# Kernel tuning notes

Measured on AMD Instinct MI355X. Metric: run time of the kernel, lower is better.

Reference implementation:

```python
import jax, jax.numpy as jnp
import numpy as np

EPS = 1e-6
NUM_HEADS = 8


def setup_inputs() -> dict:
    key0 = jax.random.key(0)
    ks = jax.random.split(key0, 8)
    N, B, C, HW = 900, 8, 256, 1156

    def lin(k):
        kw, kb = jax.random.split(k)
        W = jax.random.normal(kw, (C, C), jnp.float32) * 0.02
        b = jax.random.normal(kb, (C,), jnp.float32) * 0.02
        return W, b

    Wq, bq = lin(ks[0])
    Wk, bk = lin(ks[1])
    Wv, bv = lin(ks[2])
    Wo, bo = lin(ks[3])
    query = jax.random.normal(ks[4], (N, B, C), jnp.float32)
    key = jax.random.normal(ks[5], (HW, B, C), jnp.float32)
    query_pos = jax.random.normal(ks[6], (N, B, C), jnp.float32)
    key_pos = jax.random.normal(ks[7], (HW, B, C), jnp.float32)
    return dict(query=query, key=key, query_pos=query_pos, key_pos=key_pos,
                Wq=Wq, bq=bq, Wk=Wk, bk=bk, Wv=Wv, bv=bv, Wo=Wo, bo=bo)


def reference(query, key, query_pos, key_pos, Wq, bq, Wk, bk, Wv, bv, Wo, bo):
    # Faithful port of LinearCrossAttention.forward (value=None -> key,
    # identity=None -> query, batch_first=False, dropout inactive).
    # NOTE: the original permutes to (B, seq, head, head_dim) but then applies
    # cumsum(dim=2) / einsums along axis 2, i.e. over the HEAD axis; we
    # reproduce that exactly.
    N, B, C = query.shape
    HW = key.shape[0]
    H = NUM_HEADS
    D = C // H

    q = (query @ Wq.T + bq) + query_pos          # (N,B,C)
    k = (key @ Wk.T + bk) + key_pos              # (HW,B,C)
    v = key @ Wv.T + bv                          # (HW,B,C)

    q = jnp.transpose(q.reshape(N, B, H, D), (1, 0, 2, 3))    # (B,N,H,D)
    k = jnp.transpose(k.reshape(HW, B, H, D), (1, 0, 2, 3))   # (B,HW,H,D)
    v = jnp.transpose(v.reshape(HW, B, H, D), (1, 0, 2, 3))   # (B,HW,H,D)

    q = jax.nn.sigmoid(q)
    k = jax.nn.sigmoid(k)

    if HW > N:  # pad queries along the sequence axis
        q = jnp.concatenate([q, jnp.zeros((B, HW - N, H, D), q.dtype)], axis=1)

    dot = lambda a, b: jnp.sum(a * b, axis=-1)   # 'nhld,nhld->nhl'

    sink_incoming = 1.0 / dot(q + EPS, jnp.cumsum(k, axis=2) + EPS)   # (B,HW,H)
    source_outgoing = 1.0 / dot(k + EPS, jnp.cumsum(q, axis=2) + EPS)
    normal = (jnp.arange(H, dtype=q.dtype) + 1.0)[None, None, :]       # (1,1,H)
    sink_incoming = sink_incoming * normal
    source_outgoing = source_outgoing * normal

    conserved_sink = dot(q + EPS, jnp.cumsum(k * source_outgoing[..., None], axis=2) + EPS) / normal
    conserved_source = dot(k + EPS, jnp.cumsum(q * sink_incoming[..., None], axis=2) + EPS) / normal
    conserved_source = jnp.clip(conserved_source, -1.0, 1.0)

    sink_allocation = jax.nn.sigmoid(conserved_sink)
    conserved_source = jnp.exp(conserved_source)
    source_competition = conserved_source / jnp.cumsum(conserved_source, axis=-1) * normal

    # causal_dot_product with cumsum over axis 2 (head axis in this layout)
    qs = q * (sink_incoming[..., None] / normal[..., None])            # (B,HW,H,D)
    kv = jnp.cumsum(jnp.einsum('blhd,blhm->blhdm', k, v * source_competition[..., None]), axis=2)
    qkv = jnp.einsum('blhd,blhdm->blhm', qs, kv)                       # (B,HW,H,D)

    out = (qkv * sink_allocation[..., None])[:, :N]                    # (B,N,H,D)
    out = jnp.swapaxes(out, 1, 2).reshape(B, N, C)                     # matches torch transpose(1,2).reshape
    out = out @ Wo.T + bo
    out = jnp.swapaxes(out, 0, 1)                                      # (N,B,C)
    return query + out
```

## Files before the change

kernel.cpp:

```cpp
#include <hip/hip_runtime.h>
#include <math.h>

#define EPSV 1e-6f
constexpr int N_ = 900, B_ = 8, C_ = 256, H_ = 8, D_ = 32;
constexpr int M_TOT = N_ * B_;
constexpr int BM  = 32;
constexpr int NBLK = M_TOT / BM;
constexpr int VS  = 272;
constexpr int OFF_AQ = 65536;
constexpr int OFF_AK = 81920;
constexpr int OFF_Q  = 98304;
constexpr int OFF_K  = OFF_Q + BM * VS * 2;
constexpr int OFF_V  = OFF_K + BM * VS * 2;
constexpr int LDS1   = OFF_V + BM * VS * 2;
constexpr int LDS2   = 81920;

typedef __attribute__((ext_vector_type(8))) short short8;
typedef __attribute__((ext_vector_type(4))) float f32x4;
typedef __attribute__((ext_vector_type(2))) float f32x2;
typedef __attribute__((ext_vector_type(2))) unsigned short us2;

__device__ __forceinline__ unsigned short f2bf(float f) {
    unsigned int u = __float_as_uint(f);
    return (unsigned short)((u + 0x7FFFu + ((u >> 16) & 1u)) >> 16);
}
__device__ __forceinline__ float bf2f(unsigned short u) {
    return __uint_as_float(((unsigned int)u) << 16);
}
__device__ __forceinline__ int swz(int row, int kElem) {
    int b = (row << 9) + (kElem << 1);
    return b ^ ((row & 7) << 4);
}
__device__ __forceinline__ float red16(float v) {
    v += __shfl_xor(v, 1); v += __shfl_xor(v, 2);
    v += __shfl_xor(v, 4); v += __shfl_xor(v, 8);
    return v;
}

__global__ __launch_bounds__(256)
void pack_w(const float* __restrict__ Wq, const float* __restrict__ Wk,
            const float* __restrict__ Wv, const float* __restrict__ Wo,
            unsigned short* __restrict__ wbf)
{
    const int i = (blockIdx.x * 256 + threadIdx.x) * 8;
    const float* src = (i < 65536) ? Wq : (i < 131072) ? Wk
                     : (i < 196608) ? Wv : Wo;
    const int off = i & 65535;
    const float4 a = *reinterpret_cast<const float4*>(src + off);
    const float4 b = *reinterpret_cast<const float4*>(src + off + 4);
    short8 p;
    p[0]=(short)f2bf(a.x); p[1]=(short)f2bf(a.y);
    p[2]=(short)f2bf(a.z); p[3]=(short)f2bf(a.w);
    p[4]=(short)f2bf(b.x); p[5]=(short)f2bf(b.y);
    p[6]=(short)f2bf(b.z); p[7]=(short)f2bf(b.w);
    *reinterpret_cast<short8*>(wbf + i) = p;
}

__device__ __forceinline__ void stageW32(const unsigned short* Wmat, int kkElem,
                                         char* wbufLds, int cw, int lane)
{
    #pragma unroll
    for (int n = 0; n < 4; ++n) {
        const int L  = n * 1024 + lane * 16;
        const int cl = L >> 7;
        const int kb = (L & 127) ^ ((cl & 7) << 4);
        const char* src = (const char*)Wmat + (size_t)(cw + cl) * 512
                        + kkElem * 2 + kb;
        __builtin_amdgcn_global_load_lds(
            (const __attribute__((address_space(1))) unsigned int*)src,
            (__attribute__((address_space(3))) unsigned int*)(wbufLds + n * 1024),
            16, 0, 0);
    }
}

__device__ __forceinline__ void step_mm32(const unsigned char* At, const char* wb,
                                          int kkA, int lrow, int kg8,
                                          f32x4 acc[2][2])
{
    #pragma unroll
    for (int kh = 0; kh < 2; ++kh) {
        const short8 a0 = *reinterpret_cast<const short8*>(At + swz(lrow,      kkA + kh*32 + kg8));
        const short8 a1 = *reinterpret_cast<const short8*>(At + swz(16 + lrow, kkA + kh*32 + kg8));
        #pragma unroll
        for (int j = 0; j < 2; ++j) {
            const int cl = j*16 + lrow;
            const short8 bfr = *reinterpret_cast<const short8*>(
                wb + cl*128 + ((kh*64 + kg8*2) ^ ((cl & 7) << 4)));
            acc[0][j] = __builtin_amdgcn_mfma_f32_16x16x32_bf16(a0, bfr, acc[0][j], 0, 0, 0);
            acc[1][j] = __builtin_amdgcn_mfma_f32_16x16x32_bf16(a1, bfr, acc[1][j], 0, 0, 0);
        }
    }
}

__global__ __launch_bounds__(512)
void fused_qkva(const float* __restrict__ query, const float* __restrict__ key,
                const float* __restrict__ qpos,  const float* __restrict__ kpos,
                const unsigned short* __restrict__ wbf,
                const float* __restrict__ bq, const float* __restrict__ bk,
                const float* __restrict__ bv,
                unsigned short* __restrict__ abf)
{
    extern __shared__ char smem[];
    char* Wb = smem;
    unsigned char* Aq = (unsigned char*)(smem + OFF_AQ);
    unsigned char* Ak = (unsigned char*)(smem + OFF_AK);
    unsigned short* q_sb = (unsigned short*)(smem + OFF_Q);
    unsigned short* k_sb = (unsigned short*)(smem + OFF_K);
    unsigned short* v_sb = (unsigned short*)(smem + OFF_V);

    const int tid = threadIdx.x;
    const int r0  = blockIdx.x * BM;
    const int wave = tid >> 6, lane = tid & 63;
    const int cw = wave * 32;
    char* mywb = Wb + wave * 8192;

    stageW32(wbf, 0, mywb, cw, lane);

    {
        const int trow = tid >> 5, k0 = (tid & 31) * 8;
        #pragma unroll
        for (int i = 0; i < 2; ++i) {
            const int row = trow + i * 16;
            const float* xr = query + (size_t)(r0 + row) * C_ + k0;
            const float4 a0 = *reinterpret_cast<const float4*>(xr);
            const float4 a1 = *reinterpret_cast<const float4*>(xr + 4);
            short8 pa;
            pa[0]=(short)f2bf(a0.x); pa[1]=(short)f2bf(a0.y);
            pa[2]=(short)f2bf(a0.z); pa[3]=(short)f2bf(a0.w);
            pa[4]=(short)f2bf(a1.x); pa[5]=(short)f2bf(a1.y);
            pa[6]=(short)f2bf(a1.z); pa[7]=(short)f2bf(a1.w);
            *reinterpret_cast<short8*>(Aq + swz(row, k0)) = pa;
            const float* kr = key + (size_t)(r0 + row) * C_ + k0;
            const float4 b0 = *reinterpret_cast<const float4*>(kr);
            const float4 b1 = *reinterpret_cast<const float4*>(kr + 4);
            short8 pb;
            pb[0]=(short)f2bf(b0.x); pb[1]=(short)f2bf(b0.y);
            pb[2]=(short)f2bf(b0.z); pb[3]=(short)f2bf(b0.w);
            pb[4]=(short)f2bf(b1.x); pb[5]=(short)f2bf(b1.y);
            pb[6]=(short)f2bf(b1.z); pb[7]=(short)f2bf(b1.w);
            *reinterpret_cast<short8*>(Ak + swz(row, k0)) = pb;
        }
    }

    const int lrow = lane & 15, kg8 = (lane >> 4) * 8;
    const int crow0 = (lane >> 4) * 4, ccol = lane & 15;

    float qp[16], kp[16], bqv[2], bkv[2], bvv[2];
    #pragma unroll
    for (int j = 0; j < 2; ++j) {
        const int ch = cw + j*16 + ccol;
        bqv[j] = bq[ch]; bkv[j] = bk[ch]; bvv[j] = bv[ch];
        #pragma unroll
        for (int rh = 0; rh < 2; ++rh)
            #pragma unroll
            for (int r_ = 0; r_ < 4; ++r_) {
                const int gr = r0 + rh*16 + crow0 + r_;
                qp[j*8+rh*4+r_] = qpos[(size_t)gr * C_ + ch];
                kp[j*8+rh*4+r_] = kpos[(size_t)gr * C_ + ch];
            }
    }

    __syncthreads();

    f32x4 qacc[2][2] = {}; f32x4 kacc[2][2] = {}; f32x4 vacc[2][2] = {};

    #pragma unroll
    for (int st = 0; st < 12; ++st) {
        if (st < 11) {
            const int nx = st + 1;
            stageW32(wbf + (nx >> 2) * 65536, (nx & 3) * 64,
                     mywb + (nx & 1) * 4096, cw, lane);
            asm volatile("s_waitcnt vmcnt(4)" ::: "memory");
        } else {
            asm volatile("s_waitcnt vmcnt(0)" ::: "memory");
        }

        const char* wb = mywb + (st & 1) * 4096;
        const int kkA = (st & 3) * 64;
        if (st < 4)      step_mm32(Aq, wb, kkA, lrow, kg8, qacc);
        else if (st < 8) step_mm32(Ak, wb, kkA, lrow, kg8, kacc);
        else             step_mm32(Ak, wb, kkA, lrow, kg8, vacc);

        if (st == 3) {
            #pragma unroll
            for (int j = 0; j < 2; ++j) {
                const int ch = cw + j*16 + ccol;
                #pragma unroll
                for (int rh = 0; rh < 2; ++rh)
                    #pragma unroll
                    for (int r_ = 0; r_ < 4; ++r_) {
                        float v = qacc[rh][j][r_] + bqv[j] + qp[j*8+rh*4+r_];
                        q_sb[(rh*16+crow0+r_)*VS + ch] = f2bf(1.f/(1.f+expf(-v)));
                    }
            }
        }
        if (st == 7) {
            #pragma unroll
            for (int j = 0; j < 2; ++j) {
                const int ch = cw + j*16 + ccol;
                #pragma unroll
                for (int rh = 0; rh < 2; ++rh)
                    #pragma unroll
                    for (int r_ = 0; r_ < 4; ++r_) {
                        float v = kacc[rh][j][r_] + bkv[j] + kp[j*8+rh*4+r_];
                        k_sb[(rh*16+crow0+r_)*VS + ch] = f2bf(1.f/(1.f+expf(-v)));
                    }
            }
        }
        if (st == 11) {
            #pragma unroll
            for (int j = 0; j < 2; ++j) {
                const int ch = cw + j*16 + ccol;
                #pragma unroll
                for (int rh = 0; rh < 2; ++rh)
                    #pragma unroll
                    for (int r_ = 0; r_ < 4; ++r_)
                        v_sb[(rh*16+crow0+r_)*VS + ch] =
                            f2bf(vacc[rh][j][r_] + bvv[j]);
            }
        }
    }

    __syncthreads();

    {
        const int loc = tid >> 4, tt = tid & 15, d0 = tt * 2;
        const int gr = r0 + loc;
        const int nn = gr >> 3, bb = gr & 7;
        const unsigned short* qr = q_sb + loc * VS + d0;
        const unsigned short* kr = k_sb + loc * VS + d0;
        const unsigned short* vr = v_sb + loc * VS + d0;
        f32x2 qh[8], kh[8], vh[8];
        #pragma unroll
        for (int h = 0; h < 8; ++h) {
            const us2 tq = *reinterpret_cast<const us2*>(qr + (h << 5));
            const us2 tk = *reinterpret_cast<const us2*>(kr + (h << 5));
            const us2 tv = *reinterpret_cast<const us2*>(vr + (h << 5));
            qh[h][0] = bf2f(tq[0]); qh[h][1] = bf2f(tq[1]);
            kh[h][0] = bf2f(tk[0]); kh[h][1] = bf2f(tk[1]);
            vh[h][0] = bf2f(tv[0]); vh[h][1] = bf2f(tv[1]);
        }

        float ir1[8], so_[8];
        {
            f32x2 ck = {0,0}, cq = {0,0};
            #pragma unroll
            for (int h = 0; h < 8; ++h) {
                float p1 = 0.f, p2 = 0.f;
                #pragma unroll
                for (int j = 0; j < 2; ++j) {
                    ck[j] += kh[h][j]; cq[j] += qh[h][j];
                    p1 += (qh[h][j] + EPSV) * (ck[j] + EPSV);
                    p2 += (kh[h][j] + EPSV) * (cq[j] + EPSV);
                }
                p1 = red16(p1); p2 = red16(p2);
                ir1[h] = 1.f / p1;
                so_[h] = (float)(h+1) / p2;
            }
        }
        float salloc[8], scomp[8];
        {
            f32x2 c2 = {0,0}, c3 = {0,0};
            float css = 0.f;
            #pragma unroll
            for (int h = 0; h < 8; ++h) {
                const float sih = (float)(h+1) * ir1[h];
                float p3 = 0.f, p4 = 0.f;
                #pragma unroll
                for (int j = 0; j < 2; ++j) {
                    c2[j] += kh[h][j] * so_[h];
                    c3[j] += qh[h][j] * sih;
                    p3 += (qh[h][j] + EPSV) * (c2[j] + EPSV);
                    p4 += (kh[h][j] + EPSV) * (c3[j] + EPSV);
                }
                p3 = red16(p3); p4 = red16(p4);
                const float inv_n = 1.f / (float)(h+1);
                salloc[h] = 1.f / (1.f + expf(-p3 * inv_n));
                const float consrc = fminf(1.f, fmaxf(-1.f, p4 * inv_n));
                const float cs = expf(consrc);
                css += cs;
                scomp[h] = cs / css * (float)(h+1);
            }
        }
        #pragma unroll
        for (int h = 0; h < 8; ++h) {
            f32x2 qs2, a2 = {0,0};
            #pragma unroll
            for (int j = 0; j < 2; ++j) qs2[j] = qh[h][j] * ir1[h];
            #pragma unroll
            for (int h2 = 0; h2 <= h; ++h2) {
                float p = 0.f;
                #pragma unroll
                for (int j = 0; j < 2; ++j) p += qs2[j] * kh[h2][j];
                p = red16(p);
                const float w = p * scomp[h2];
                #pragma unroll
                for (int j = 0; j < 2; ++j) a2[j] += w * vh[h2][j];
            }
            us2 o;
            o[0] = f2bf(a2[0] * salloc[h]);
            o[1] = f2bf(a2[1] * salloc[h]);
            *reinterpret_cast<us2*>(abf + (size_t)bb*(H_*N_*D_) + (size_t)h*(N_*D_)
                                        + (size_t)nn*D_ + d0) = o;
        }
    }
}

__global__ __launch_bounds__(512)
void outproj(const unsigned short* __restrict__ abf,
             const unsigned short* __restrict__ wbf,
             const float* __restrict__ bo,
             const float* __restrict__ query,
             float* __restrict__ out)
{
    extern __shared__ char smem[];
    char* Wb = smem;
    unsigned char* As = (unsigned char*)(smem + 65536);
    const int tid = threadIdx.x;
    const int r0  = blockIdx.x * BM;
    const int wave = tid >> 6, lane = tid & 63;
    const int cw = wave * 32;
    char* mywb = Wb + wave * 8192;
    const unsigned short* Wo = wbf + 3*65536;

    stageW32(Wo, 0, mywb, cw, lane);

    {
        const int trow = tid >> 5, k0 = (tid & 31) * 8;
        #pragma unroll
        for (int i = 0; i < 2; ++i) {
            const int row = trow + i * 16;
            const int gr = r0 + row;
            const int nn = gr >> 3, bb = gr & 7;
            const short8 p = *reinterpret_cast<const short8*>(
                abf + (size_t)bb * (N_*C_) + (size_t)nn * C_ + k0);
            *reinterpret_cast<short8*>(As + swz(row, k0)) = p;
        }
    }

    const int lrow = lane & 15, kg8 = (lane >> 4) * 8;
    const int crow0 = (lane >> 4) * 4, ccol = lane & 15;

    float bov[2], qres[16];
    #pragma unroll
    for (int j = 0; j < 2; ++j) {
        const int ch = cw + j*16 + ccol;
        bov[j] = bo[ch];
        #pragma unroll
        for (int rh = 0; rh < 2; ++rh)
            #pragma unroll
            for (int r_ = 0; r_ < 4; ++r_)
                qres[j*8+rh*4+r_] =
                    query[(size_t)(r0 + rh*16 + crow0 + r_) * C_ + ch];
    }

    __syncthreads();

    f32x4 acc[2][2] = {};
    #pragma unroll
    for (int sp = 0; sp < 4; ++sp) {
        if (sp < 3) {
            stageW32(Wo, (sp+1)*64, mywb + ((sp+1) & 1) * 4096, cw, lane);
            asm volatile("s_waitcnt vmcnt(4)" ::: "memory");
        } else {
            asm volatile("s_waitcnt vmcnt(0)" ::: "memory");
        }
        step_mm32(As, mywb + (sp & 1) * 4096, sp*64, lrow, kg8, acc);
    }

    #pragma unroll
    for (int j = 0; j < 2; ++j) {
        const int ch = cw + j*16 + ccol;
        #pragma unroll
        for (int rh = 0; rh < 2; ++rh)
            #pragma unroll
            for (int r_ = 0; r_ < 4; ++r_) {
                const size_t g = (size_t)(r0 + rh*16 + crow0 + r_) * C_ + ch;
                out[g] = acc[rh][j][r_] + bov[j] + qres[j*8+rh*4+r_];
            }
    }
}

extern "C" void kernel_launch(void* const* d_in, const int* in_sizes, int n_in,
                              void* d_out, int out_size, void* d_ws, size_t ws_size,
                              hipStream_t stream)
{
    const float* query = (const float*)d_in[0];
    const float* key   = (const float*)d_in[1];
    const float* qpos  = (const float*)d_in[2];
    const float* kpos  = (const float*)d_in[3];
    const float* Wq = (const float*)d_in[4];  const float* bq = (const float*)d_in[5];
    const float* Wk = (const float*)d_in[6];  const float* bk = (const float*)d_in[7];
    const float* Wv = (const float*)d_in[8];  const float* bv = (const float*)d_in[9];
    const float* Wo = (const float*)d_in[10]; const float* bo = (const float*)d_in[11];

    unsigned short* wbf = (unsigned short*)d_ws;
    unsigned short* abf = wbf + 4*65536;
    float* out = (float*)d_out;

    pack_w<<<128, 256, 0, stream>>>(Wq, Wk, Wv, Wo, wbf);
    fused_qkva<<<NBLK, 512, LDS1, stream>>>(query, key, qpos, kpos, wbf,
                                            bq, bk, bv, abf);
    outproj<<<NBLK, 512, LDS2, stream>>>(abf, wbf, bo, query, out);
}
```

Baseline: 34.26 us.

## Drop weight pre-pack kernel; stream fp32 weights and convert to bf16 in-loop

Removes the separate pack_w launch that converted all four weight matrices to bf16, and instead streams fp32 weights directly into LDS and converts them to bf16 right before each MFMA. This saves one kernel launch and the write and re-read of the packed weights. In exchange, every block re-converts weights redundantly, fetches twice the weight bytes per k-step, and the K loop runs twice as many stages with half the work per stage.

Result: slower. 46.77 us (+36.5%).

```diff
diff --git a/kernel.cpp b/kernel.cpp
--- a/kernel.cpp
+++ b/kernel.cpp
@@ -37,35 +37,15 @@
     return v;
 }
 
-__global__ __launch_bounds__(256)
-void pack_w(const float* __restrict__ Wq, const float* __restrict__ Wk,
-            const float* __restrict__ Wv, const float* __restrict__ Wo,
-            unsigned short* __restrict__ wbf)
-{
-    const int i = (blockIdx.x * 256 + threadIdx.x) * 8;
-    const float* src = (i < 65536) ? Wq : (i < 131072) ? Wk
-                     : (i < 196608) ? Wv : Wo;
-    const int off = i & 65535;
-    const float4 a = *reinterpret_cast<const float4*>(src + off);
-    const float4 b = *reinterpret_cast<const float4*>(src + off + 4);
-    short8 p;
-    p[0]=(short)f2bf(a.x); p[1]=(short)f2bf(a.y);
-    p[2]=(short)f2bf(a.z); p[3]=(short)f2bf(a.w);
-    p[4]=(short)f2bf(b.x); p[5]=(short)f2bf(b.y);
-    p[6]=(short)f2bf(b.z); p[7]=(short)f2bf(b.w);
-    *reinterpret_cast<short8*>(wbf + i) = p;
-}
-
-__device__ __forceinline__ void stageW32(const unsigned short* Wmat, int kkElem,
-                                         char* wbufLds, int cw, int lane)
+__device__ __forceinline__ void stageW32f(const float* Wmat, int kk32,
+                                          char* wbufLds, int cw, int lane)
 {
     #pragma unroll
     for (int n = 0; n < 4; ++n) {
         const int L  = n * 1024 + lane * 16;
         const int cl = L >> 7;
         const int kb = (L & 127) ^ ((cl & 7) << 4);
-        const char* src = (const char*)Wmat + (size_t)(cw + cl) * 512
-                        + kkElem * 2 + kb;
+        const char* src = (const char*)(Wmat + (size_t)(cw + cl) * C_ + kk32) + kb;
         __builtin_amdgcn_global_load_lds(
             (const __attribute__((address_space(1))) unsigned int*)src,
             (__attribute__((address_space(3))) unsigned int*)(wbufLds + n * 1024),
@@ -73,29 +53,33 @@
     }
 }
 
-__device__ __forceinline__ void step_mm32(const unsigned char* At, const char* wb,
-                                          int kkA, int lrow, int kg8,
-                                          f32x4 acc[2][2])
-{
-    #pragma unroll
-    for (int kh = 0; kh < 2; ++kh) {
-        const short8 a0 = *reinterpret_cast<const short8*>(At + swz(lrow,      kkA + kh*32 + kg8));
-        const short8 a1 = *reinterpret_cast<const short8*>(At + swz(16 + lrow, kkA + kh*32 + kg8));
-        #pragma unroll
-        for (int j = 0; j < 2; ++j) {
-            const int cl = j*16 + lrow;
-            const short8 bfr = *reinterpret_cast<const short8*>(
-                wb + cl*128 + ((kh*64 + kg8*2) ^ ((cl & 7) << 4)));
-            acc[0][j] = __builtin_amdgcn_mfma_f32_16x16x32_bf16(a0, bfr, acc[0][j], 0, 0, 0);
-            acc[1][j] = __builtin_amdgcn_mfma_f32_16x16x32_bf16(a1, bfr, acc[1][j], 0, 0, 0);
-        }
+__device__ __forceinline__ void step_mmf(const unsigned char* At, const char* wb,
+                                         int kkA, int lrow, int kg8,
+                                         f32x4 acc[2][2])
+{
+    const short8 a0 = *reinterpret_cast<const short8*>(At + swz(lrow,      kkA + kg8));
+    const short8 a1 = *reinterpret_cast<const short8*>(At + swz(16 + lrow, kkA + kg8));
+    #pragma unroll
+    for (int j = 0; j < 2; ++j) {
+        const int cl = j*16 + lrow;
+        const int o0 = (kg8 * 4) ^ ((cl & 7) << 4);
+        const float4 w0 = *reinterpret_cast<const float4*>(wb + cl*128 + o0);
+        const float4 w1 = *reinterpret_cast<const float4*>(wb + cl*128 + (o0 ^ 16));
+        short8 bfr;
+        bfr[0]=(short)f2bf(w0.x); bfr[1]=(short)f2bf(w0.y);
+        bfr[2]=(short)f2bf(w0.z); bfr[3]=(short)f2bf(w0.w);
+        bfr[4]=(short)f2bf(w1.x); bfr[5]=(short)f2bf(w1.y);
+        bfr[6]=(short)f2bf(w1.z); bfr[7]=(short)f2bf(w1.w);
+        acc[0][j] = __builtin_amdgcn_mfma_f32_16x16x32_bf16(a0, bfr, acc[0][j], 0, 0, 0);
+        acc[1][j] = __builtin_amdgcn_mfma_f32_16x16x32_bf16(a1, bfr, acc[1][j], 0, 0, 0);
     }
 }
 
 __global__ __launch_bounds__(512)
 void fused_qkva(const float* __restrict__ query, const float* __restrict__ key,
                 const float* __restrict__ qpos,  const float* __restrict__ kpos,
-                const unsigned short* __restrict__ wbf,
+                const float* __restrict__ Wq, const float* __restrict__ Wk,
+                const float* __restrict__ Wv,
                 const float* __restrict__ bq, const float* __restrict__ bk,
                 const float* __restrict__ bv,
                 unsigned short* __restrict__ abf)
@@ -114,7 +98,7 @@
     const int cw = wave * 32;
     char* mywb = Wb + wave * 8192;
 
-    stageW32(wbf, 0, mywb, cw, lane);
+    stageW32f(Wq, 0, mywb, cw, lane);
 
     {
         const int trow = tid >> 5, k0 = (tid & 31) * 8;
@@ -165,23 +149,23 @@
     f32x4 qacc[2][2] = {}; f32x4 kacc[2][2] = {}; f32x4 vacc[2][2] = {};
 
     #pragma unroll
-    for (int st = 0; st < 12; ++st) {
-        if (st < 11) {
+    for (int st = 0; st < 24; ++st) {
+        if (st < 23) {
             const int nx = st + 1;
-            stageW32(wbf + (nx >> 2) * 65536, (nx & 3) * 64,
-                     mywb + (nx & 1) * 4096, cw, lane);
+            const float* Wm = (nx < 8) ? Wq : (nx < 16) ? Wk : Wv;
+            stageW32f(Wm, (nx & 7) * 32, mywb + (nx & 1) * 4096, cw, lane);
             asm volatile("s_waitcnt vmcnt(4)" ::: "memory");
         } else {
             asm volatile("s_waitcnt vmcnt(0)" ::: "memory");
         }
 
         const char* wb = mywb + (st & 1) * 4096;
-        const int kkA = (st & 3) * 64;
-        if (st < 4)      step_mm32(Aq, wb, kkA, lrow, kg8, qacc);
-        else if (st < 8) step_mm32(Ak, wb, kkA, lrow, kg8, kacc);
-        else             step_mm32(Ak, wb, kkA, lrow, kg8, vacc);
-
-        if (st == 3) {
+        const int kkA = (st & 7) * 32;
+        if (st < 8)       step_mmf(Aq, wb, kkA, lrow, kg8, qacc);
+        else if (st < 16) step_mmf(Ak, wb, kkA, lrow, kg8, kacc);
+        else              step_mmf(Ak, wb, kkA, lrow, kg8, vacc);
+
+        if (st == 7) {
             #pragma unroll
             for (int j = 0; j < 2; ++j) {
                 const int ch = cw + j*16 + ccol;
@@ -194,7 +178,7 @@
                     }
             }
         }
-        if (st == 7) {
+        if (st == 15) {
             #pragma unroll
             for (int j = 0; j < 2; ++j) {
                 const int ch = cw + j*16 + ccol;
@@ -207,7 +191,7 @@
                     }
             }
         }
-        if (st == 11) {
+        if (st == 23) {
             #pragma unroll
             for (int j = 0; j < 2; ++j) {
                 const int ch = cw + j*16 + ccol;
@@ -308,7 +292,7 @@
 
 __global__ __launch_bounds__(512)
 void outproj(const unsigned short* __restrict__ abf,
-             const unsigned short* __restrict__ wbf,
+             const float* __restrict__ Wo,
              const float* __restrict__ bo,
              const float* __restrict__ query,
              float* __restrict__ out)
@@ -321,9 +305,8 @@
     const int wave = tid >> 6, lane = tid & 63;
     const int cw = wave * 32;
     char* mywb = Wb + wave * 8192;
-    const unsigned short* Wo = wbf + 3*65536;
-
-    stageW32(Wo, 0, mywb, cw, lane);
+
+    stageW32f(Wo, 0, mywb, cw, lane);
 
     {
         const int trow = tid >> 5, k0 = (tid & 31) * 8;
@@ -358,14 +341,14 @@
 
     f32x4 acc[2][2] = {};
     #pragma unroll
-    for (int sp = 0; sp < 4; ++sp) {
-        if (sp < 3) {
-            stageW32(Wo, (sp+1)*64, mywb + ((sp+1) & 1) * 4096, cw, lane);
+    for (int sp = 0; sp < 8; ++sp) {
+        if (sp < 7) {
+            stageW32f(Wo, (sp+1)*32, mywb + ((sp+1) & 1) * 4096, cw, lane);
             asm volatile("s_waitcnt vmcnt(4)" ::: "memory");
         } else {
             asm volatile("s_waitcnt vmcnt(0)" ::: "memory");
         }
-        step_mm32(As, mywb + (sp & 1) * 4096, sp*64, lrow, kg8, acc);
+        step_mmf(As, mywb + (sp & 1) * 4096, sp*32, lrow, kg8, acc);
     }
 
     #pragma unroll
@@ -394,12 +377,10 @@
     const float* Wv = (const float*)d_in[8];  const float* bv = (const float*)d_in[9];
     const float* Wo = (const float*)d_in[10]; const float* bo = (const float*)d_in[11];
 
-    unsigned short* wbf = (unsigned short*)d_ws;
-    unsigned short* abf = wbf + 4*65536;
+    unsigned short* abf = (unsigned short*)d_ws;
     float* out = (float*)d_out;
 
-    pack_w<<<128, 256, 0, stream>>>(Wq, Wk, Wv, Wo, wbf);
-    fused_qkva<<<NBLK, 512, LDS1, stream>>>(query, key, qpos, kpos, wbf,
-                                            bq, bk, bv, abf);
-    outproj<<<NBLK, 512, LDS2, stream>>>(abf, wbf, bo, query, out);
-}
+    fused_qkva<<<NBLK, 512, LDS1, stream>>>(query, key, qpos, kpos,
+                                            Wq, Wk, Wv, bq, bk, bv, abf);
+    outproj<<<NBLK, 512, LDS2, stream>>>(abf, Wo, bo, query, out);
+}
```
